# Optimization experiments

Measured on AMD Instinct MI355X. Metric: run time of the kernel, lower is better.

## Reference

```python
import jax, jax.numpy as jnp
import numpy as np

N_HEADS = 16


def setup_inputs() -> dict:
    key = jax.random.key(0)
    ks = jax.random.split(key, 5)
    B, S, D = 2, 2048, 1024
    H = N_HEADS
    return {
        "queries": jax.random.normal(ks[0], (B, S, D), dtype=jnp.float32),
        "keys": jax.random.normal(ks[1], (B, S, D), dtype=jnp.float32),
        "values": jax.random.normal(ks[2], (B, S, D), dtype=jnp.float32),
        "bias": jax.random.normal(ks[3], (1, H, S, S), dtype=jnp.float32) * 0.02,
        "w_out": jax.random.normal(ks[4], (D, D), dtype=jnp.float32) * (1.0 / np.sqrt(D)),
    }


def _split_heads(x, n_heads):
    B, S, D = x.shape
    return x.reshape(B, S, n_heads, D // n_heads).transpose(0, 2, 1, 3)  # [B,H,S,hd]


def reference(queries, keys, values, bias, w_out):
    H = N_HEADS
    q = _split_heads(queries, H)
    k = _split_heads(keys, H)
    v = _split_heads(values, H)
    hd = k.shape[-1]
    # NOTE: original adds bias to raw logits, THEN scales by 1/sqrt(dk)
    logits = jnp.einsum("bhqd,bhkd->bhqk", q, k) + bias
    weights = jax.nn.softmax(logits * (1.0 / np.sqrt(hd)), axis=-1)
    attn = jnp.einsum("bhqk,bhkd->bhqd", weights, v)  # [B,H,Sq,hd]
    B, _, Sq, _ = attn.shape
    combined = attn.transpose(0, 2, 1, 3).reshape(B, Sq, H * hd)
    return combined @ w_out
```

## Files before the change

kernel.cpp:

```cpp
#include <hip/hip_runtime.h>

typedef float  f32x4  __attribute__((ext_vector_type(4)));
typedef short  bf16x8 __attribute__((ext_vector_type(8)));
typedef short  s16x4  __attribute__((ext_vector_type(4)));
typedef unsigned int u32x4 __attribute__((ext_vector_type(4)));

#define MFMA_BF16 __builtin_amdgcn_mfma_f32_16x16x32_bf16

__device__ __forceinline__ short f2bf(float f) {
  __bf16 h = (__bf16)f;
  return __builtin_bit_cast(short, h);
}

constexpr int S = 2048, D = 1024, H = 16, HD = 64;
constexpr int NT = S / 64;
constexpr float SCALE = 0.125f;
constexpr float L2E = 1.44269504f;
constexpr float SL = SCALE * L2E;

#define GLDS16(g, l) __builtin_amdgcn_global_load_lds( \
    (const __attribute__((address_space(1))) unsigned*)(g), \
    (__attribute__((address_space(3))) unsigned*)(l), 16, 0, 0)

#define WAITV(n) asm volatile("s_waitcnt vmcnt(" #n ")" ::: "memory")
#define SBAR()   __builtin_amdgcn_s_barrier()

__global__ __launch_bounds__(256)
void kv_prep(const float* __restrict__ Kg, const float* __restrict__ Vg,
             short* __restrict__ Kb, short* __restrict__ Vb) {
  const int tile = blockIdx.x, h = blockIdx.y, b = blockIdx.z;
  const int t = threadIdx.x, lane = t & 63, w = t >> 6;
  const int lg = lane >> 4, lm = lane & 15;
  __shared__ short kt[64 * 68], vt[64 * 68];
  const float* kp = Kg + ((size_t)(b * S + tile * 64)) * D + h * HD;
  const float* vp = Vg + ((size_t)(b * S + tile * 64)) * D + h * HD;
  #pragma unroll
  for (int i = 0; i < 4; ++i) {
    int idx = i * 256 + t, r = idx >> 4, c4 = (idx & 15) * 4;
    float4 k4 = *(const float4*)(kp + (size_t)r * D + c4);
    s16x4 ks; ks[0]=f2bf(k4.x); ks[1]=f2bf(k4.y); ks[2]=f2bf(k4.z); ks[3]=f2bf(k4.w);
    *(s16x4*)&kt[r * 68 + c4] = ks;
    float4 v4 = *(const float4*)(vp + (size_t)r * D + c4);
    s16x4 vs; vs[0]=f2bf(v4.x); vs[1]=f2bf(v4.y); vs[2]=f2bf(v4.z); vs[3]=f2bf(v4.w);
    *(s16x4*)&vt[r * 68 + c4] = vs;
  }
  __syncthreads();
  const size_t obase = ((size_t)((b * H + h) * NT + tile)) * 4096;
  #pragma unroll
  for (int j = 0; j < 2; ++j) {
    int f = w + j * 4, kk = f >> 2, mf = f & 3;
    int row = mf * 16 + lm, col = kk * 32 + lg * 4;
    s16x4 c0 = *(const s16x4*)&kt[row * 68 + col];
    s16x4 c1 = *(const s16x4*)&kt[row * 68 + col + 16];
    bf16x8 a;
    a[0]=c0[0]; a[1]=c0[1]; a[2]=c0[2]; a[3]=c0[3];
    a[4]=c1[0]; a[5]=c1[1]; a[6]=c1[2]; a[7]=c1[3];
    *(bf16x8*)&Kb[obase + (size_t)(f * 64 + lane) * 8] = a;
  }
  #pragma unroll
  for (int j = 0; j < 2; ++j) {
    int f = w + j * 4, kk = f >> 2, of = f & 3;
    int col = of * 16 + lm;
    bf16x8 a;
    #pragma unroll
    for (int half = 0; half < 2; ++half)
      #pragma unroll
      for (int e = 0; e < 4; ++e)
        a[half * 4 + e] = vt[(kk * 32 + lg * 4 + half * 16 + e) * 68 + col];
    *(bf16x8*)&Vb[obase + (size_t)(f * 64 + lane) * 8] = a;
  }
}

__device__ __forceinline__ void attn_tile(const short* kb, const short* vb,
                                          const f32x4 (&br)[2][4],
                                          const bf16x8 (&qf)[2][2],
                                          int lane, float* M, float* L,
                                          f32x4 (&o)[2][4]) {
  const f32x4 zero4 = {0.f, 0.f, 0.f, 0.f};
  f32x4 sacc[2][4];
  #pragma unroll
  for (int fq = 0; fq < 2; ++fq)
    #pragma unroll
    for (int i = 0; i < 4; ++i) sacc[fq][i] = zero4;
  __builtin_amdgcn_s_setprio(1);
  #pragma unroll
  for (int kk = 0; kk < 2; ++kk)
    #pragma unroll
    for (int mf = 0; mf < 4; ++mf) {
      bf16x8 a = *(const bf16x8*)&kb[(kk * 4 + mf) * 512 + lane * 8];
      sacc[0][mf] = MFMA_BF16(a, qf[0][kk], sacc[0][mf], 0, 0, 0);
      sacc[1][mf] = MFMA_BF16(a, qf[1][kk], sacc[1][mf], 0, 0, 0);
    }
  __builtin_amdgcn_s_setprio(0);
  float p[2][4][4];
  float tmax[2] = {-__builtin_inff(), -__builtin_inff()};
  #pragma unroll
  for (int fq = 0; fq < 2; ++fq)
    #pragma unroll
    for (int mf = 0; mf < 4; ++mf)
      #pragma unroll
      for (int j = 0; j < 4; ++j) {
        float tv = (sacc[fq][mf][j] + br[fq][mf][j]) * SL;
        p[fq][mf][j] = tv;
        tmax[fq] = fmaxf(tmax[fq], tv);
      }
  #pragma unroll
  for (int fq = 0; fq < 2; ++fq) {
    tmax[fq] = fmaxf(tmax[fq], __shfl_xor(tmax[fq], 16, 64));
    tmax[fq] = fmaxf(tmax[fq], __shfl_xor(tmax[fq], 32, 64));
  }
  const int skip = (tmax[0] <= M[0]) && (tmax[1] <= M[1]);
  if (!__all(skip)) {
    #pragma unroll
    for (int fq = 0; fq < 2; ++fq) {
      float Mn = fmaxf(M[fq], tmax[fq]);
      float alpha = exp2f(M[fq] - Mn);
      #pragma unroll
      for (int of = 0; of < 4; ++of) {
        o[fq][of][0] *= alpha; o[fq][of][1] *= alpha;
        o[fq][of][2] *= alpha; o[fq][of][3] *= alpha;
      }
      L[fq] *= alpha;
      M[fq] = Mn;
    }
  }
  #pragma unroll
  for (int fq = 0; fq < 2; ++fq) {
    float psum = 0.f;
    #pragma unroll
    for (int mf = 0; mf < 4; ++mf)
      #pragma unroll
      for (int j = 0; j < 4; ++j) {
        float e = exp2f(p[fq][mf][j] - M[fq]);
        p[fq][mf][j] = e;
        psum += e;
      }
    psum += __shfl_xor(psum, 16, 64);
    psum += __shfl_xor(psum, 32, 64);
    L[fq] += psum;
  }
  bf16x8 pb[2][2];
  #pragma unroll
  for (int fq = 0; fq < 2; ++fq)
    #pragma unroll
    for (int kk = 0; kk < 2; ++kk)
      #pragma unroll
      for (int j = 0; j < 8; ++j)
        pb[fq][kk][j] = f2bf(p[fq][kk * 2 + (j >> 2)][j & 3]);
  __builtin_amdgcn_s_setprio(1);
  #pragma unroll
  for (int kk = 0; kk < 2; ++kk)
    #pragma unroll
    for (int of = 0; of < 4; ++of) {
      bf16x8 a = *(const bf16x8*)&vb[(kk * 4 + of) * 512 + lane * 8];
      o[0][of] = MFMA_BF16(a, pb[0][kk], o[0][of], 0, 0, 0);
      o[1][of] = MFMA_BF16(a, pb[1][kk], o[1][of], 0, 0, 0);
    }
  __builtin_amdgcn_s_setprio(0);
}

__global__ __launch_bounds__(128, 2)
void attn_fused(const float* __restrict__ Qg, const float* __restrict__ Bg,
                const short* __restrict__ Kb, const short* __restrict__ Vb,
                short* __restrict__ comb) {
  __shared__ __attribute__((aligned(16))) short smem[16384];
  const int bid = blockIdx.x;
  const int x = bid & 15, rr = bid >> 4;
  const int c = x & 7, b = x >> 3;
  const int h = rr >> 2, qt = (rr & 3) * 8 + c;
  const int q0 = qt * 64;
  const int t = threadIdx.x, lane = t & 63, w = t >> 6;
  const int lg = lane >> 4, lm = lane & 15;

  bf16x8 qf[2][2];
  #pragma unroll
  for (int fq = 0; fq < 2; ++fq) {
    const float* qp = Qg + ((size_t)(b * S + q0 + w * 32 + fq * 16 + lm)) * D + h * HD;
    #pragma unroll
    for (int kk = 0; kk < 2; ++kk)
      #pragma unroll
      for (int j = 0; j < 8; ++j)
        qf[fq][kk][j] = f2bf(qp[kk * 32 + (j >> 2) * 16 + lg * 4 + (j & 3)]);
  }

  const short* Kt = Kb + ((size_t)(b * H + h) * NT) * 4096;
  const short* Vt = Vb + ((size_t)(b * H + h) * NT) * 4096;
  const float* bp = Bg + ((size_t)(h * S + q0 + w * 32 + lm)) * S + lg * 4;

  const f32x4 zero4 = {0.f, 0.f, 0.f, 0.f};
  f32x4 o[2][4];
  #pragma unroll
  for (int fq = 0; fq < 2; ++fq)
    #pragma unroll
    for (int i = 0; i < 4; ++i) o[fq][i] = zero4;
  float M[2] = {-__builtin_inff(), -__builtin_inff()};
  float L[2] = {0.f, 0.f};

#define STAGE(tile, buf)                                                \
  {                                                                     \
    const short* kg_ = Kt + (size_t)(tile) * 4096;                      \
    const short* vg_ = Vt + (size_t)(tile) * 4096;                      \
    _Pragma("unroll")                                                   \
    for (int f_ = 0; f_ < 4; ++f_) {                                    \
      int fr_ = w * 4 + f_;                                             \
      GLDS16(kg_ + (size_t)(fr_ * 64 + lane) * 8, (buf) + fr_ * 512);   \
      GLDS16(vg_ + (size_t)(fr_ * 64 + lane) * 8, (buf) + 4096 + fr_ * 512); \
    }                                                                   \
  }

#define BLOAD(dst, tile)                                                \
  {                                                                     \
    _Pragma("unroll")                                                   \
    for (int fq_ = 0; fq_ < 2; ++fq_)                                   \
      _Pragma("unroll")                                                 \
      for (int mf_ = 0; mf_ < 4; ++mf_)                                 \
        dst[fq_][mf_] = *(const f32x4*)(bp + (size_t)fq_ * 16 * S +     \
                                        (size_t)(tile) * 64 + mf_ * 16); \
  }

  f32x4 biasA[2][4], biasB[2][4];
  BLOAD(biasA, 0);
  STAGE(0, smem);
  BLOAD(biasB, 1);

  for (int tt = 0; tt < NT; tt += 2) {
    SBAR();
    STAGE(tt + 1, smem + 8192);
    WAITV(16);
    SBAR();
    attn_tile(smem, smem + 4096, biasA, qf, lane, M, L, o);
    { int bt = (tt + 2 < NT) ? tt + 2 : 0; BLOAD(biasA, bt); }
    SBAR();
    { int st = (tt + 2 < NT) ? tt + 2 : 0; STAGE(st, smem); }
    WAITV(16);
    SBAR();
    attn_tile(smem + 8192, smem + 12288, biasB, qf, lane, M, L, o);
    { int bt = (tt + 3 < NT) ? tt + 3 : 1; BLOAD(biasB, bt); }
  }

  const float iL0 = 1.f / L[0], iL1 = 1.f / L[1];
  __syncthreads();
  short* out_lds = smem;
  #pragma unroll
  for (int fq = 0; fq < 2; ++fq)
    #pragma unroll
    for (int of = 0; of < 4; ++of)
      #pragma unroll
      for (int j = 0; j < 4; ++j)
        out_lds[(w * 32 + fq * 16 + lm) * 72 + of * 16 + lg * 4 + j] =
            f2bf(o[fq][of][j] * (fq ? iL1 : iL0));
  __syncthreads();
  #pragma unroll
  for (int it = 0; it < 4; ++it) {
    int idx = it * 128 + t;
    int r = idx >> 3, seg = idx & 7;
    u32x4 u = *(const u32x4*)&out_lds[r * 72 + seg * 8];
    *(u32x4*)&comb[((size_t)(b * S + q0 + r)) * D + h * HD + seg * 8] = u;
  }
#undef STAGE
#undef BLOAD
}

__global__ __launch_bounds__(256)
void wt_kernel(const float* __restrict__ W, short* __restrict__ Wt) {
  __shared__ __attribute__((aligned(16))) short tile[64 * 72];
  const int n0 = blockIdx.x * 64, k0 = blockIdx.y * 64;
  const int t = threadIdx.x;
  #pragma unroll
  for (int i = 0; i < 4; ++i) {
    int idx = i * 256 + t;
    int r  = idx >> 4, c4 = (idx & 15) * 4;
    float4 wv = *(const float4*)(W + (size_t)(k0 + r) * D + n0 + c4);
    tile[(c4 + 0) * 72 + r] = f2bf(wv.x);
    tile[(c4 + 1) * 72 + r] = f2bf(wv.y);
    tile[(c4 + 2) * 72 + r] = f2bf(wv.z);
    tile[(c4 + 3) * 72 + r] = f2bf(wv.w);
  }
  __syncthreads();
  #pragma unroll
  for (int it = 0; it < 2; ++it) {
    int idx = it * 256 + t;
    int r = idx >> 3, seg = idx & 7;
    u32x4 u = *(const u32x4*)&tile[r * 72 + seg * 8];
    *(u32x4*)&Wt[(size_t)(n0 + r) * D + k0 + seg * 8] = u;
  }
}

__device__ __forceinline__ bf16x8 ld_frag_swz(const short* base, int row, int kk, int lg) {
  const char* rp = (const char*)base + row * 128 + (lg & 1) * 8;
  int u0 = kk * 4 + (lg >> 1);
  int f  = row & 7;
  s16x4 c0 = *(const s16x4*)(rp + ((u0 ^ f) << 4));
  s16x4 c1 = *(const s16x4*)(rp + (((u0 + 2) ^ f) << 4));
  bf16x8 a;
  a[0]=c0[0]; a[1]=c0[1]; a[2]=c0[2]; a[3]=c0[3];
  a[4]=c1[0]; a[5]=c1[1]; a[6]=c1[2]; a[7]=c1[3];
  return a;
}

__global__ __launch_bounds__(256, 2)
void proj_gemm(const short* __restrict__ A, const short* __restrict__ Bt,
               float* __restrict__ C) {
  __shared__ __attribute__((aligned(16))) short a_lds[2][8192];
  __shared__ __attribute__((aligned(16))) short b_lds[2][4096];
  const int m0 = blockIdx.x * 128, n0 = blockIdx.y * 64;
  const int t = threadIdx.x, lane = t & 63, w = t >> 6;
  const int lg = lane >> 4, lm = lane & 15;
  const int srow = lane >> 3;
  const int sunit = (lane & 7) ^ srow;

  const f32x4 zero4 = {0.f, 0.f, 0.f, 0.f};
  f32x4 acc[2][4];
  #pragma unroll
  for (int i = 0; i < 2; ++i)
    #pragma unroll
    for (int j = 0; j < 4; ++j) acc[i][j] = zero4;

#define PSTAGE(ks, ab, bb)                                                  \
  {                                                                         \
    const short* ag_ = A  + (size_t)m0 * D + (ks) * 64;                     \
    const short* bg_ = Bt + (size_t)n0 * D + (ks) * 64;                     \
    _Pragma("unroll")                                                       \
    for (int i_ = 0; i_ < 4; ++i_) {                                        \
      int j_ = w * 4 + i_;                                                  \
      GLDS16(ag_ + (size_t)(j_ * 8 + srow) * D + sunit * 8, (ab) + j_ * 512); \
    }                                                                       \
    _Pragma("unroll")                                                       \
    for (int i_ = 0; i_ < 2; ++i_) {                                        \
      int j_ = w * 2 + i_;                                                  \
      GLDS16(bg_ + (size_t)(j_ * 8 + srow) * D + sunit * 8, (bb) + j_ * 512); \
    }                                                                       \
  }

#define PCOMPUTE(ab, bb)                                                    \
  {                                                                         \
    _Pragma("unroll")                                                       \
    for (int kk = 0; kk < 2; ++kk) {                                        \
      bf16x8 af0 = ld_frag_swz(ab, w * 32 + lm, kk, lg);                    \
      bf16x8 af1 = ld_frag_swz(ab, w * 32 + 16 + lm, kk, lg);               \
      bf16x8 bf0 = ld_frag_swz(bb, lm, kk, lg);                             \
      bf16x8 bf1 = ld_frag_swz(bb, 16 + lm, kk, lg);                        \
      bf16x8 bf2 = ld_frag_swz(bb, 32 + lm, kk, lg);                        \
      bf16x8 bf3 = ld_frag_swz(bb, 48 + lm, kk, lg);                        \
      __builtin_amdgcn_s_setprio(1);                                        \
      acc[0][0] = MFMA_BF16(af0, bf0, acc[0][0], 0, 0, 0);                  \
      acc[0][1] = MFMA_BF16(af0, bf1, acc[0][1], 0, 0, 0);                  \
      acc[0][2] = MFMA_BF16(af0, bf2, acc[0][2], 0, 0, 0);                  \
      acc[0][3] = MFMA_BF16(af0, bf3, acc[0][3], 0, 0, 0);                  \
      acc[1][0] = MFMA_BF16(af1, bf0, acc[1][0], 0, 0, 0);                  \
      acc[1][1] = MFMA_BF16(af1, bf1, acc[1][1], 0, 0, 0);                  \
      acc[1][2] = MFMA_BF16(af1, bf2, acc[1][2], 0, 0, 0);                  \
      acc[1][3] = MFMA_BF16(af1, bf3, acc[1][3], 0, 0, 0);                  \
      __builtin_amdgcn_s_setprio(0);                                        \
    }                                                                       \
  }

  PSTAGE(0, a_lds[0], b_lds[0]);
  for (int ks = 0; ks < 16; ks += 2) {
    SBAR();
    PSTAGE(ks + 1, a_lds[1], b_lds[1]);
    WAITV(6);
    SBAR();
    PCOMPUTE(a_lds[0], b_lds[0]);
    SBAR();
    if (ks + 2 < 16) {
      PSTAGE(ks + 2, a_lds[0], b_lds[0]);
      WAITV(6);
    } else {
      WAITV(0);
    }
    SBAR();
    PCOMPUTE(a_lds[1], b_lds[1]);
  }

  #pragma unroll
  for (int mf = 0; mf < 2; ++mf)
    #pragma unroll
    for (int j = 0; j < 4; ++j)
      #pragma unroll
      for (int nf = 0; nf < 4; ++nf)
        C[(size_t)(m0 + w * 32 + mf * 16 + lg * 4 + j) * D +
          n0 + nf * 16 + lm] = acc[mf][nf][j];
#undef PSTAGE
#undef PCOMPUTE
}

extern "C" void kernel_launch(void* const* d_in, const int* in_sizes, int n_in,
                              void* d_out, int out_size, void* d_ws, size_t ws_size,
                              hipStream_t stream) {
  const float* Qg = (const float*)d_in[0];
  const float* Kg = (const float*)d_in[1];
  const float* Vg = (const float*)d_in[2];
  const float* Bg = (const float*)d_in[3];
  const float* Wg = (const float*)d_in[4];
  float* out = (float*)d_out;

  short* comb = (short*)d_ws;
  short* Wt   = comb + (size_t)(2 * S) * D;
  short* Kb   = Wt   + (size_t)D * D;
  short* Vb   = Kb   + (size_t)2 * H * NT * 4096;

  kv_prep<<<dim3(NT, H, 2), 256, 0, stream>>>(Kg, Vg, Kb, Vb);
  wt_kernel<<<dim3(D / 64, D / 64), 256, 0, stream>>>(Wg, Wt);
  attn_fused<<<dim3(1024), 128, 0, stream>>>(Qg, Bg, Kb, Vb, comb);
  proj_gemm<<<dim3(32, 16), 256, 0, stream>>>(comb, Wt, out);
}
```

Baseline: 154.8 us.

## Split attention KV range across blocks and merge partials in a combine kernel

Each attention block now handles 128 queries with 256 threads and only half of the key range (split-K), writing unnormalized fp32 partial outputs plus per-row max and sum. A new combine kernel merges the two halves with log-sum-exp rescaling and writes the bf16 combined tensor. K and V tiles are interleaved into one buffer so a single staging loop loads both. Bias is loaded directly into the score accumulator instead of being added after the matmul. The schedule goes from two-tile unrolling to a single-tile double-buffered loop. This aims for more blocks per CU and shorter serial loops, at the cost of an extra kernel launch and an fp32 partial round trip through global memory.

```diff
diff --git a/kernel.cpp b/kernel.cpp
--- a/kernel.cpp
+++ b/kernel.cpp
@@ -14,6 +14,7 @@
 
 constexpr int S = 2048, D = 1024, H = 16, HD = 64;
 constexpr int NT = S / 64;
+constexpr int NTH = 16;
 constexpr float SCALE = 0.125f;
 constexpr float L2E = 1.44269504f;
 constexpr float SL = SCALE * L2E;
@@ -27,7 +28,7 @@
 
 __global__ __launch_bounds__(256)
 void kv_prep(const float* __restrict__ Kg, const float* __restrict__ Vg,
-             short* __restrict__ Kb, short* __restrict__ Vb) {
+             short* __restrict__ KVb) {
   const int tile = blockIdx.x, h = blockIdx.y, b = blockIdx.z;
   const int t = threadIdx.x, lane = t & 63, w = t >> 6;
   const int lg = lane >> 4, lm = lane & 15;
@@ -45,7 +46,7 @@
     *(s16x4*)&vt[r * 68 + c4] = vs;
   }
   __syncthreads();
-  const size_t obase = ((size_t)((b * H + h) * NT + tile)) * 4096;
+  const size_t obase = ((size_t)((b * H + h) * NT + tile)) * 8192;
   #pragma unroll
   for (int j = 0; j < 2; ++j) {
     int f = w + j * 4, kk = f >> 2, mf = f & 3;
@@ -55,11 +56,11 @@
     bf16x8 a;
     a[0]=c0[0]; a[1]=c0[1]; a[2]=c0[2]; a[3]=c0[3];
     a[4]=c1[0]; a[5]=c1[1]; a[6]=c1[2]; a[7]=c1[3];
-    *(bf16x8*)&Kb[obase + (size_t)(f * 64 + lane) * 8] = a;
+    *(bf16x8*)&KVb[obase + (size_t)(f * 64 + lane) * 8] = a;
   }
   #pragma unroll
   for (int j = 0; j < 2; ++j) {
-    int f = w + j * 4, kk = f >> 2, of = f & 3;
+    int fv = w + j * 4, kk = fv >> 2, of = fv & 3;
     int col = of * 16 + lm;
     bf16x8 a;
     #pragma unroll
@@ -67,108 +68,22 @@
       #pragma unroll
       for (int e = 0; e < 4; ++e)
         a[half * 4 + e] = vt[(kk * 32 + lg * 4 + half * 16 + e) * 68 + col];
-    *(bf16x8*)&Vb[obase + (size_t)(f * 64 + lane) * 8] = a;
-  }
-}
-
-__device__ __forceinline__ void attn_tile(const short* kb, const short* vb,
-                                          const f32x4 (&br)[2][4],
-                                          const bf16x8 (&qf)[2][2],
-                                          int lane, float* M, float* L,
-                                          f32x4 (&o)[2][4]) {
-  const f32x4 zero4 = {0.f, 0.f, 0.f, 0.f};
-  f32x4 sacc[2][4];
-  #pragma unroll
-  for (int fq = 0; fq < 2; ++fq)
-    #pragma unroll
-    for (int i = 0; i < 4; ++i) sacc[fq][i] = zero4;
-  __builtin_amdgcn_s_setprio(1);
-  #pragma unroll
-  for (int kk = 0; kk < 2; ++kk)
-    #pragma unroll
-    for (int mf = 0; mf < 4; ++mf) {
-      bf16x8 a = *(const bf16x8*)&kb[(kk * 4 + mf) * 512 + lane * 8];
-      sacc[0][mf] = MFMA_BF16(a, qf[0][kk], sacc[0][mf], 0, 0, 0);
-      sacc[1][mf] = MFMA_BF16(a, qf[1][kk], sacc[1][mf], 0, 0, 0);
-    }
-  __builtin_amdgcn_s_setprio(0);
-  float p[2][4][4];
-  float tmax[2] = {-__builtin_inff(), -__builtin_inff()};
-  #pragma unroll
-  for (int fq = 0; fq < 2; ++fq)
-    #pragma unroll
-    for (int mf = 0; mf < 4; ++mf)
-      #pragma unroll
-      for (int j = 0; j < 4; ++j) {
-        float tv = (sacc[fq][mf][j] + br[fq][mf][j]) * SL;
-        p[fq][mf][j] = tv;
-        tmax[fq] = fmaxf(tmax[fq], tv);
-      }
-  #pragma unroll
-  for (int fq = 0; fq < 2; ++fq) {
-    tmax[fq] = fmaxf(tmax[fq], __shfl_xor(tmax[fq], 16, 64));
-    tmax[fq] = fmaxf(tmax[fq], __shfl_xor(tmax[fq], 32, 64));
-  }
-  const int skip = (tmax[0] <= M[0]) && (tmax[1] <= M[1]);
-  if (!__all(skip)) {
-    #pragma unroll
-    for (int fq = 0; fq < 2; ++fq) {
-      float Mn = fmaxf(M[fq], tmax[fq]);
-      float alpha = exp2f(M[fq] - Mn);
-      #pragma unroll
-      for (int of = 0; of < 4; ++of) {
-        o[fq][of][0] *= alpha; o[fq][of][1] *= alpha;
-        o[fq][of][2] *= alpha; o[fq][of][3] *= alpha;
-      }
-      L[fq] *= alpha;
-      M[fq] = Mn;
-    }
-  }
-  #pragma unroll
-  for (int fq = 0; fq < 2; ++fq) {
-    float psum = 0.f;
-    #pragma unroll
-    for (int mf = 0; mf < 4; ++mf)
-      #pragma unroll
-      for (int j = 0; j < 4; ++j) {
-        float e = exp2f(p[fq][mf][j] - M[fq]);
-        p[fq][mf][j] = e;
-        psum += e;
-      }
-    psum += __shfl_xor(psum, 16, 64);
-    psum += __shfl_xor(psum, 32, 64);
-    L[fq] += psum;
-  }
-  bf16x8 pb[2][2];
-  #pragma unroll
-  for (int fq = 0; fq < 2; ++fq)
-    #pragma unroll
-    for (int kk = 0; kk < 2; ++kk)
-      #pragma unroll
-      for (int j = 0; j < 8; ++j)
-        pb[fq][kk][j] = f2bf(p[fq][kk * 2 + (j >> 2)][j & 3]);
-  __builtin_amdgcn_s_setprio(1);
-  #pragma unroll
-  for (int kk = 0; kk < 2; ++kk)
-    #pragma unroll
-    for (int of = 0; of < 4; ++of) {
-      bf16x8 a = *(const bf16x8*)&vb[(kk * 4 + of) * 512 + lane * 8];
-      o[0][of] = MFMA_BF16(a, pb[0][kk], o[0][of], 0, 0, 0);
-      o[1][of] = MFMA_BF16(a, pb[1][kk], o[1][of], 0, 0, 0);
-    }
-  __builtin_amdgcn_s_setprio(0);
-}
-
-__global__ __launch_bounds__(128, 2)
+    *(bf16x8*)&KVb[obase + (size_t)((8 + fv) * 64 + lane) * 8] = a;
+  }
+}
+
+__global__ __launch_bounds__(256, 3)
 void attn_fused(const float* __restrict__ Qg, const float* __restrict__ Bg,
-                const short* __restrict__ Kb, const short* __restrict__ Vb,
-                short* __restrict__ comb) {
+                const short* __restrict__ KVb,
+                float* __restrict__ OP, float* __restrict__ ML) {
   __shared__ __attribute__((aligned(16))) short smem[16384];
   const int bid = blockIdx.x;
-  const int x = bid & 15, rr = bid >> 4;
-  const int c = x & 7, b = x >> 3;
-  const int h = rr >> 2, qt = (rr & 3) * 8 + c;
-  const int q0 = qt * 64;
+  const int c = bid & 7, g = bid >> 3;
+  const int qb = g & 15, z = g >> 4;
+  const int h = (c << 1) | (z & 1);
+  const int b = (z >> 1) & 1;
+  const int half = z >> 2;
+  const int q0 = qb * 128;
   const int t = threadIdx.x, lane = t & 63, w = t >> 6;
   const int lg = lane >> 4, lm = lane & 15;
 
@@ -183,9 +98,8 @@
         qf[fq][kk][j] = f2bf(qp[kk * 32 + (j >> 2) * 16 + lg * 4 + (j & 3)]);
   }
 
-  const short* Kt = Kb + ((size_t)(b * H + h) * NT) * 4096;
-  const short* Vt = Vb + ((size_t)(b * H + h) * NT) * 4096;
-  const float* bp = Bg + ((size_t)(h * S + q0 + w * 32 + lm)) * S + lg * 4;
+  const short* KVt = KVb + ((size_t)((b * H + h) * NT + half * NTH)) * 8192;
+  const float* bp = Bg + ((size_t)(h * S + q0 + w * 32 + lm)) * S + half * 1024 + lg * 4;
 
   const f32x4 zero4 = {0.f, 0.f, 0.f, 0.f};
   f32x4 o[2][4];
@@ -195,70 +109,167 @@
     for (int i = 0; i < 4; ++i) o[fq][i] = zero4;
   float M[2] = {-__builtin_inff(), -__builtin_inff()};
   float L[2] = {0.f, 0.f};
+  f32x4 sacc[2][4];
 
 #define STAGE(tile, buf)                                                \
   {                                                                     \
-    const short* kg_ = Kt + (size_t)(tile) * 4096;                      \
-    const short* vg_ = Vt + (size_t)(tile) * 4096;                      \
+    const short* kvg_ = KVt + (size_t)(tile) * 8192;                    \
     _Pragma("unroll")                                                   \
     for (int f_ = 0; f_ < 4; ++f_) {                                    \
       int fr_ = w * 4 + f_;                                             \
-      GLDS16(kg_ + (size_t)(fr_ * 64 + lane) * 8, (buf) + fr_ * 512);   \
-      GLDS16(vg_ + (size_t)(fr_ * 64 + lane) * 8, (buf) + 4096 + fr_ * 512); \
+      GLDS16(kvg_ + (size_t)(fr_ * 64 + lane) * 8, (buf) + fr_ * 512);  \
     }                                                                   \
   }
 
-#define BLOAD(dst, tile)                                                \
+#define BLOAD(tile)                                                     \
   {                                                                     \
     _Pragma("unroll")                                                   \
     for (int fq_ = 0; fq_ < 2; ++fq_)                                   \
       _Pragma("unroll")                                                 \
       for (int mf_ = 0; mf_ < 4; ++mf_)                                 \
-        dst[fq_][mf_] = *(const f32x4*)(bp + (size_t)fq_ * 16 * S +     \
-                                        (size_t)(tile) * 64 + mf_ * 16); \
-  }
-
-  f32x4 biasA[2][4], biasB[2][4];
-  BLOAD(biasA, 0);
+        sacc[fq_][mf_] = *(const f32x4*)(bp + (size_t)fq_ * 16 * S +    \
+                                         (size_t)(tile) * 64 + mf_ * 16); \
+  }
+
   STAGE(0, smem);
-  BLOAD(biasB, 1);
-
-  for (int tt = 0; tt < NT; tt += 2) {
-    SBAR();
-    STAGE(tt + 1, smem + 8192);
-    WAITV(16);
-    SBAR();
-    attn_tile(smem, smem + 4096, biasA, qf, lane, M, L, o);
-    { int bt = (tt + 2 < NT) ? tt + 2 : 0; BLOAD(biasA, bt); }
-    SBAR();
-    { int st = (tt + 2 < NT) ? tt + 2 : 0; STAGE(st, smem); }
-    WAITV(16);
-    SBAR();
-    attn_tile(smem + 8192, smem + 12288, biasB, qf, lane, M, L, o);
-    { int bt = (tt + 3 < NT) ? tt + 3 : 1; BLOAD(biasB, bt); }
-  }
-
-  const float iL0 = 1.f / L[0], iL1 = 1.f / L[1];
-  __syncthreads();
-  short* out_lds = smem;
+  BLOAD(0);
+
+  for (int tt = 0; tt < NTH; ++tt) {
+    SBAR();
+    if (tt < NTH - 1) {
+      STAGE(tt + 1, smem + ((tt + 1) & 1) * 8192);
+      WAITV(12);
+    } else {
+      WAITV(8);
+    }
+    SBAR();
+    const short* buf = smem + (tt & 1) * 8192;
+
+    __builtin_amdgcn_s_setprio(1);
+    #pragma unroll
+    for (int kk = 0; kk < 2; ++kk)
+      #pragma unroll
+      for (int mf = 0; mf < 4; ++mf) {
+        bf16x8 a = *(const bf16x8*)&buf[(kk * 4 + mf) * 512 + lane * 8];
+        sacc[0][mf] = MFMA_BF16(a, qf[0][kk], sacc[0][mf], 0, 0, 0);
+        sacc[1][mf] = MFMA_BF16(a, qf[1][kk], sacc[1][mf], 0, 0, 0);
+      }
+    __builtin_amdgcn_s_setprio(0);
+
+    float tmax[2] = {-__builtin_inff(), -__builtin_inff()};
+    #pragma unroll
+    for (int fq = 0; fq < 2; ++fq)
+      #pragma unroll
+      for (int mf = 0; mf < 4; ++mf)
+        #pragma unroll
+        for (int j = 0; j < 4; ++j) {
+          float tv = sacc[fq][mf][j] * SL;
+          sacc[fq][mf][j] = tv;
+          tmax[fq] = fmaxf(tmax[fq], tv);
+        }
+    #pragma unroll
+    for (int fq = 0; fq < 2; ++fq) {
+      tmax[fq] = fmaxf(tmax[fq], __shfl_xor(tmax[fq], 16, 64));
+      tmax[fq] = fmaxf(tmax[fq], __shfl_xor(tmax[fq], 32, 64));
+    }
+    const int skip = (tmax[0] <= M[0]) && (tmax[1] <= M[1]);
+    if (!__all(skip)) {
+      #pragma unroll
+      for (int fq = 0; fq < 2; ++fq) {
+        float Mn = fmaxf(M[fq], tmax[fq]);
+        float alpha = exp2f(M[fq] - Mn);
+        #pragma unroll
+        for (int of = 0; of < 4; ++of) {
+          o[fq][of][0] *= alpha; o[fq][of][1] *= alpha;
+          o[fq][of][2] *= alpha; o[fq][of][3] *= alpha;
+        }
+        L[fq] *= alpha;
+        M[fq] = Mn;
+      }
+    }
+    #pragma unroll
+    for (int fq = 0; fq < 2; ++fq) {
+      float psum = 0.f;
+      #pragma unroll
+      for (int mf = 0; mf < 4; ++mf)
+        #pragma unroll
+        for (int j = 0; j < 4; ++j) {
+          float e = exp2f(sacc[fq][mf][j] - M[fq]);
+          sacc[fq][mf][j] = e;
+          psum += e;
+        }
+      psum += __shfl_xor(psum, 16, 64);
+      psum += __shfl_xor(psum, 32, 64);
+      L[fq] += psum;
+    }
+    bf16x8 pb[2][2];
+    #pragma unroll
+    for (int fq = 0; fq < 2; ++fq)
+      #pragma unroll
+      for (int kk = 0; kk < 2; ++kk)
+        #pragma unroll
+        for (int j = 0; j < 8; ++j)
+          pb[fq][kk][j] = f2bf(sacc[fq][kk * 2 + (j >> 2)][j & 3]);
+
+    if (tt < NTH - 1) BLOAD(tt + 1);
+
+    __builtin_amdgcn_s_setprio(1);
+    #pragma unroll
+    for (int kk = 0; kk < 2; ++kk)
+      #pragma unroll
+      for (int of = 0; of < 4; ++of) {
+        bf16x8 a = *(const bf16x8*)&buf[4096 + (kk * 4 + of) * 512 + lane * 8];
+        o[0][of] = MFMA_BF16(a, pb[0][kk], o[0][of], 0, 0, 0);
+        o[1][of] = MFMA_BF16(a, pb[1][kk], o[1][of], 0, 0, 0);
+      }
+    __builtin_amdgcn_s_setprio(0);
+  }
+
+  const int p = ((b * H + h) << 4) | qb;
+  float* opb = OP + ((size_t)(half * 512 + p)) * 8192;
   #pragma unroll
   for (int fq = 0; fq < 2; ++fq)
     #pragma unroll
     for (int of = 0; of < 4; ++of)
-      #pragma unroll
-      for (int j = 0; j < 4; ++j)
-        out_lds[(w * 32 + fq * 16 + lm) * 72 + of * 16 + lg * 4 + j] =
-            f2bf(o[fq][of][j] * (fq ? iL1 : iL0));
-  __syncthreads();
-  #pragma unroll
-  for (int it = 0; it < 4; ++it) {
-    int idx = it * 128 + t;
-    int r = idx >> 3, seg = idx & 7;
-    u32x4 u = *(const u32x4*)&out_lds[r * 72 + seg * 8];
-    *(u32x4*)&comb[((size_t)(b * S + q0 + r)) * D + h * HD + seg * 8] = u;
+      *(f32x4*)&opb[(w * 32 + fq * 16 + lm) * 64 + of * 16 + lg * 4] = o[fq][of];
+  float* mlb = ML + ((size_t)(half * 512 + p)) * 256;
+  if (lane < 16) {
+    mlb[w * 32 + lm]        = M[0];
+    mlb[w * 32 + 16 + lm]   = M[1];
+    mlb[128 + w * 32 + lm]      = L[0];
+    mlb[128 + w * 32 + 16 + lm] = L[1];
   }
 #undef STAGE
 #undef BLOAD
+}
+
+__global__ __launch_bounds__(256)
+void combine(const float* __restrict__ OP, const float* __restrict__ ML,
+             short* __restrict__ comb) {
+  const int p = blockIdx.x;
+  const int b = p >> 8, h = (p >> 4) & 15, qb = p & 15;
+  const int t = threadIdx.x;
+  const float* o1 = OP + (size_t)p * 8192;
+  const float* o2 = OP + (size_t)(512 + p) * 8192;
+  const float* m1p = ML + (size_t)p * 256;
+  const float* m2p = ML + (size_t)(512 + p) * 256;
+  #pragma unroll
+  for (int k = 0; k < 8; ++k) {
+    int e = (k * 256 + t) * 4;
+    int q = e >> 6, d = e & 63;
+    f32x4 a = *(const f32x4*)&o1[e];
+    f32x4 c = *(const f32x4*)&o2[e];
+    float m1 = m1p[q], m2 = m2p[q];
+    float l1 = m1p[128 + q], l2 = m2p[128 + q];
+    float m = fmaxf(m1, m2);
+    float a1 = exp2f(m1 - m), a2 = exp2f(m2 - m);
+    float inv = 1.f / (l1 * a1 + l2 * a2);
+    s16x4 r;
+    #pragma unroll
+    for (int j = 0; j < 4; ++j)
+      r[j] = f2bf((a[j] * a1 + c[j] * a2) * inv);
+    *(s16x4*)&comb[((size_t)(b * S + qb * 128 + q)) * D + h * HD + d] = r;
+  }
 }
 
 __global__ __launch_bounds__(256)
@@ -396,12 +407,14 @@
   float* out = (float*)d_out;
 
   short* comb = (short*)d_ws;
-  short* Wt   = comb + (size_t)(2 * S) * D;
-  short* Kb   = Wt   + (size_t)D * D;
-  short* Vb   = Kb   + (size_t)2 * H * NT * 4096;
-
-  kv_prep<<<dim3(NT, H, 2), 256, 0, stream>>>(Kg, Vg, Kb, Vb);
+  short* Wt   = comb + (size_t)4096 * 1024;
+  short* KVb  = Wt   + (size_t)1024 * 1024;
+  float* OP   = (float*)(KVb + (size_t)2 * H * NT * 8192);
+  float* ML   = OP + (size_t)2 * 512 * 8192;
+
+  kv_prep<<<dim3(NT, H, 2), 256, 0, stream>>>(Kg, Vg, KVb);
   wt_kernel<<<dim3(D / 64, D / 64), 256, 0, stream>>>(Wg, Wt);
-  attn_fused<<<dim3(1024), 128, 0, stream>>>(Qg, Bg, Kb, Vb, comb);
+  attn_fused<<<dim3(1024), 256, 0, stream>>>(Qg, Bg, KVb, OP, ML);
+  combine<<<dim3(512), 256, 0, stream>>>(OP, ML, comb);
   proj_gemm<<<dim3(32, 16), 256, 0, stream>>>(comb, Wt, out);
 }
```

After: 168.4 us. 8.8% more time.
